# Optimization experiments

Measured on AMD Instinct MI355X. Metric: run time of the kernel, lower is better.

## Reference

```python
import jax, jax.numpy as jnp
import numpy as np

NTASKS = 10
CAP = 8
L = 256
D_IN = 768
D_DOWN = 768
B = 64
NUM_ITERS = 3


def squash(t, axis=-1, eps=1e-16):
    sq = jnp.sum(t * t, axis=axis, keepdims=True) + eps
    return (sq / (1.0 + sq)) * t / jnp.sqrt(sq)


def setup_inputs() -> dict:
    key = jax.random.key(0)
    ks = jax.random.split(key, 8)
    return {
        "x": jax.random.normal(ks[0], (B, L, D_IN), jnp.float32),
        "fc1_w": jax.random.normal(ks[1], (NTASKS, D_DOWN, D_IN), jnp.float32) * 0.02,
        "fc1_b": jax.random.normal(ks[2], (NTASKS, D_DOWN), jnp.float32) * 0.02,
        "fc2_w": jax.random.normal(ks[3], (NTASKS, CAP, D_DOWN), jnp.float32) * 0.02,
        "fc2_b": jax.random.normal(ks[4], (NTASKS, CAP), jnp.float32) * 0.02,
        "route_weights": jax.random.normal(ks[5], (CAP, NTASKS, L * CAP, L), jnp.float32),
        "larger_w": jax.random.normal(ks[6], (NTASKS, D_DOWN, CAP), jnp.float32) * 0.02,
        "larger_b": jax.random.normal(ks[7], (NTASKS, D_DOWN), jnp.float32) * 0.02,
        "eval_t": 5,
    }


def reference(x, fc1_w, fc1_b, fc2_w, fc2_b, route_weights, larger_w, larger_b, eval_t):
    # ---- semantic capsules: per-task two-layer MLP ----
    # h1: [T, B, L, D_DOWN]; h2: [T, B, L, CAP]
    h1 = jnp.einsum("bli,tdi->tbld", x, fc1_w) + fc1_b[:, None, None, :]
    h2 = jnp.einsum("tbld,tcd->tblc", h1, fc2_w) + fc2_b[:, None, None, :]
    # torch: per-task view(B, L*CAP, 1) then cat on last dim -> [B, L*CAP, T]
    sem = jnp.transpose(h2.reshape(NTASKS, B, L * CAP), (1, 2, 0))
    sem = squash(sem, axis=-1)            # squash over task dim (dim=-1)
    sem = jnp.transpose(sem, (0, 2, 1))   # [B, T, L*CAP]

    # ---- tsv capsules: dynamic routing ----
    # priors: [CAP, B, T, class_dim=L]  (singleton dim of torch version dropped)
    priors = jnp.einsum("bri,crio->cbro", sem, route_weights)
    tsv_row = (jnp.arange(NTASKS) <= eval_t).astype(priors.dtype)   # tril row
    mask = jnp.where(tsv_row > 0, 0.0, -10000.0).astype(priors.dtype)
    logits = jnp.zeros_like(priors)
    vote = None
    for i in range(NUM_ITERS):
        logits = logits * tsv_row[None, None, :, None] + mask[None, None, :, None]
        probs = jax.nn.softmax(logits, axis=2)               # over routes (tasks)
        vote = jnp.sum(probs * priors, axis=2, keepdims=True)  # [CAP, B, 1, L]
        out = squash(vote, axis=-1)
        if i != NUM_ITERS - 1:
            logits = logits + jnp.sum(priors * out, axis=-1, keepdims=True)

    # torch raw view: [CAP, B, 1, 1, L] flat -> (B, L, CAP)
    h = vote.reshape(B, L, CAP)
    h = jnp.einsum("blc,dc->bld", h, larger_w[eval_t]) + larger_b[eval_t]
    return h


if __name__ == "__main__":
    out = reference(**setup_inputs())
    print(out.shape)
```

## Files before the change

### kernel.cpp

```cpp
#include <hip/hip_runtime.h>

constexpr int NT = 10;
constexpr int CP = 8;
constexpr int LLn = 256;
constexpr int DI = 768;
constexpr int DD = 768;
constexpr int BB = 64;
constexpr int BLr = BB * LLn;
constexpr int RR = LLn * CP;

__global__ __launch_bounds__(256) void k_w12(const float* __restrict__ w1,
                                             const float* __restrict__ w2,
                                             float* __restrict__ w12) {
  const int t = blockIdx.y;
  const int i0 = blockIdx.x * 64;
  __shared__ float sW1[64][68];
  __shared__ float sW2[CP][64];
  const int tid = threadIdx.x;
  const int il = tid >> 2;
  const int cc = (tid & 3) * 2;
  float a0 = 0.f, a1 = 0.f;
  for (int d0 = 0; d0 < DD; d0 += 64) {
#pragma unroll
    for (int p = 0; p < 4; p++) {
      int idx = p * 256 + tid;
      int dl = idx >> 4, c4 = (idx & 15) * 4;
      *(float4*)&sW1[dl][c4] =
          *(const float4*)(w1 + ((size_t)t * DD + d0 + dl) * DI + i0 + c4);
    }
    if (tid < 128) {
      int c = tid >> 4, d4 = (tid & 15) * 4;
      *(float4*)&sW2[c][d4] =
          *(const float4*)(w2 + ((size_t)t * CP + c) * DD + d0 + d4);
    }
    __syncthreads();
#pragma unroll 16
    for (int dl = 0; dl < 64; ++dl) {
      float v = sW1[dl][il];
      a0 += v * sW2[cc][dl];
      a1 += v * sW2[cc + 1][dl];
    }
    __syncthreads();
  }
  w12[((size_t)t * CP + cc) * DI + i0 + il]     = a0;
  w12[((size_t)t * CP + cc + 1) * DI + i0 + il] = a1;
}

__global__ __launch_bounds__(128) void k_b12(const float* __restrict__ b1,
                                             const float* __restrict__ w2,
                                             const float* __restrict__ b2,
                                             float* __restrict__ b12) {
  int tc = threadIdx.x;
  if (tc >= NT * CP) return;
  int t = tc >> 3, c = tc & 7;
  float s = b2[t * CP + c];
  const float* b1r = b1 + (size_t)t * DD;
  const float* w2r = w2 + ((size_t)t * CP + c) * DD;
  for (int d = 0; d < DD; ++d) s += b1r[d] * w2r[d];
  b12[tc] = s;
}

__global__ __launch_bounds__(256) void k_fc(const float* __restrict__ x,
                                            const float* __restrict__ w12,
                                            const float* __restrict__ b12,
                                            float* __restrict__ h2) {
  const int m0 = blockIdx.x * 64;
  const int tid = threadIdx.x;
  const int q = tid & 7;
  const int mg = tid >> 3;
  const float4* x4 = (const float4*)x;
  const float4* w4 = (const float4*)w12;
  const float4* xr0 = x4 + (size_t)(m0 + 2 * mg) * (DI / 4);
  const float4* xr1 = xr0 + (DI / 4);
  const float4* wr = w4 + (size_t)(q * 10) * (DI / 4);
  float acc0[10], acc1[10];
#pragma unroll
  for (int k = 0; k < 10; ++k) { acc0[k] = 0.f; acc1[k] = 0.f; }
#pragma unroll 2
  for (int i4 = 0; i4 < DI / 4; ++i4) {
    float4 xv0 = xr0[i4];
    float4 xv1 = xr1[i4];
#pragma unroll
    for (int k = 0; k < 10; ++k) {
      float4 wv = wr[(size_t)k * (DI / 4) + i4];
      acc0[k] += xv0.x * wv.x + xv0.y * wv.y + xv0.z * wv.z + xv0.w * wv.w;
      acc1[k] += xv1.x * wv.x + xv1.y * wv.y + xv1.z * wv.z + xv1.w * wv.w;
    }
  }
#pragma unroll
  for (int k = 0; k < 10; ++k) {
    int tc = q * 10 + k;
    int t = tc >> 3, c = tc & 7;
    float bv = b12[tc];
    h2[((size_t)t * BLr + m0 + 2 * mg + 0) * CP + c] = acc0[k] + bv;
    h2[((size_t)t * BLr + m0 + 2 * mg + 1) * CP + c] = acc1[k] + bv;
  }
}

__global__ __launch_bounds__(256) void k_squash_sem(const float* __restrict__ h2,
                                                    const int* __restrict__ etp,
                                                    float* __restrict__ sems) {
  int et = *etp;
  int i = blockIdx.x * 256 + threadIdx.x;
  if (i >= BB * RR) return;
  float v[NT];
  float sq = 0.f;
#pragma unroll
  for (int t = 0; t < NT; ++t) {
    v[t] = h2[(size_t)t * BB * RR + i];
    sq += v[t] * v[t];
  }
  sq += 1e-16f;
  float scale = (sq / (1.f + sq)) * rsqrtf(sq);
#pragma unroll
  for (int t = 0; t < NT; ++t)
    if (t <= et) sems[(size_t)t * BB * RR + i] = scale * v[t];
}

constexpr int OT = 64;
constexpr int RK = 64;
__global__ __launch_bounds__(256) void k_priors(const float* __restrict__ sems,
                                                const float* __restrict__ rw,
                                                const int* __restrict__ etp,
                                                float* __restrict__ priors) {
  int et = *etp;
  int t = blockIdx.y;
  if (t > et) return;
  int c2 = blockIdx.z;
  int o0 = blockIdx.x * OT;
  int tid = threadIdx.x;
  __shared__ float semT[RK][BB + 4];
  __shared__ float rwS[RK][OT + 4];
  int og = (tid & 15) * 4;
  int bg = (tid >> 4) * 4;
  float acc[4][4] = {};
  for (int r0 = 0; r0 < RR; r0 += RK) {
#pragma unroll
    for (int p = 0; p < 4; p++) {
      int idx = p * 256 + tid;
      int b = idx >> 4;
      int r4 = (idx & 15) * 4;
      float4 v = *(const float4*)(sems + ((size_t)t * BB + b) * RR + r0 + r4);
      semT[r4 + 0][b] = v.x; semT[r4 + 1][b] = v.y;
      semT[r4 + 2][b] = v.z; semT[r4 + 3][b] = v.w;
    }
#pragma unroll
    for (int p = 0; p < 4; p++) {
      int idx = p * 256 + tid;
      int r = idx >> 4;
      int o4 = (idx & 15) * 4;
      *(float4*)&rwS[r][o4] =
          *(const float4*)(rw + ((size_t)(c2 * NT + t) * RR + r0 + r) * LLn + o0 + o4);
    }
    __syncthreads();
#pragma unroll 8
    for (int r = 0; r < RK; ++r) {
      float4 a = *(const float4*)&semT[r][bg];
      float4 w = *(const float4*)&rwS[r][og];
#pragma unroll
      for (int i = 0; i < 4; i++)
#pragma unroll
        for (int j = 0; j < 4; j++) acc[i][j] += a[i] * w[j];
    }
    __syncthreads();
  }
#pragma unroll
  for (int i = 0; i < 4; i++)
#pragma unroll
    for (int j = 0; j < 4; j++)
      priors[((size_t)(c2 * NT + t) * BB + bg + i) * LLn + o0 + og + j] = acc[i][j];
}

__global__ __launch_bounds__(256) void k_route(const float* __restrict__ priors,
                                               const int* __restrict__ etp,
                                               float* __restrict__ h) {
  int et = *etp;
  int b = blockIdx.x, c2 = blockIdx.y;
  int o = threadIdx.x;
  __shared__ float pri[NT][LLn];
  __shared__ float rbuf[256];
  for (int t = 0; t <= et; ++t)
    pri[t][o] = priors[((size_t)(c2 * NT + t) * BB + b) * LLn + o];
  __syncthreads();
  float Lg[NT];
#pragma unroll
  for (int t = 0; t < NT; ++t) Lg[t] = 0.f;
  float vote = 0.f;
  for (int it = 0; it < 3; ++it) {
    float mx = -1e30f;
    for (int t = 0; t <= et; ++t) mx = fmaxf(mx, Lg[t]);
    float p[NT];
    float s = 0.f;
    for (int t = 0; t <= et; ++t) { p[t] = expf(Lg[t] - mx); s += p[t]; }
    float inv = 1.f / s;
    vote = 0.f;
    for (int t = 0; t <= et; ++t) vote += p[t] * inv * pri[t][o];
    if (it == 2) break;
    rbuf[o] = vote * vote;
    __syncthreads();
    for (int st = 128; st > 0; st >>= 1) {
      if (o < st) rbuf[o] += rbuf[o + st];
      __syncthreads();
    }
    float sq = rbuf[0] + 1e-16f;
    __syncthreads();
    float scale = (sq / (1.f + sq)) * rsqrtf(sq);
    for (int t = 0; t <= et; ++t) {
      rbuf[o] = pri[t][o] * vote;
      __syncthreads();
      for (int st = 128; st > 0; st >>= 1) {
        if (o < st) rbuf[o] += rbuf[o + st];
        __syncthreads();
      }
      Lg[t] += scale * rbuf[0];
      __syncthreads();
    }
  }
  h[((size_t)c2 * BB + b) * LLn + o] = vote;
}

__global__ __launch_bounds__(256) void k_out(const float* __restrict__ h,
                                             const float* __restrict__ lw,
                                             const float* __restrict__ lb,
                                             const int* __restrict__ etp,
                                             float* __restrict__ out) {
  int et = *etp;
  int row = blockIdx.x;
  const float* hr = h + (size_t)row * CP;
  float hv[CP];
#pragma unroll
  for (int c = 0; c < CP; ++c) hv[c] = hr[c];
  const float* lwb = lw + (size_t)et * DD * CP;
  const float* lbb = lb + (size_t)et * DD;
  for (int d = threadIdx.x; d < DD; d += 256) {
    const float* w = lwb + (size_t)d * CP;
    float s2 = lbb[d];
#pragma unroll
    for (int c = 0; c < CP; ++c) s2 += hv[c] * w[c];
    out[(size_t)row * DD + d] = s2;
  }
}

extern "C" void kernel_launch(void* const* d_in, const int* in_sizes, int n_in,
                              void* d_out, int out_size, void* d_ws, size_t ws_size,
                              hipStream_t stream) {
  const float* x  = (const float*)d_in[0];
  const float* w1 = (const float*)d_in[1];
  const float* b1 = (const float*)d_in[2];
  const float* w2 = (const float*)d_in[3];
  const float* b2 = (const float*)d_in[4];
  const float* rw = (const float*)d_in[5];
  const float* lw = (const float*)d_in[6];
  const float* lb = (const float*)d_in[7];
  const int* etp  = (const int*)d_in[8];
  float* out = (float*)d_out;

  char* ws = (char*)d_ws;
  size_t off = 0;
  auto alloc = [&](size_t bytes) {
    void* p = ws + off;
    off = (off + bytes + 255) & ~(size_t)255;
    return p;
  };
  float* w12   = (float*)alloc((size_t)NT * CP * DI * 4);
  float* b12   = (float*)alloc((size_t)NT * CP * 4);
  float* h2    = (float*)alloc((size_t)NT * BLr * CP * 4);
  float* sems  = (float*)alloc((size_t)NT * BB * RR * 4);
  float* priors= (float*)alloc((size_t)CP * NT * BB * LLn * 4);
  float* hbuf  = (float*)alloc((size_t)CP * BB * LLn * 4);

  k_w12<<<dim3(DI / 64, NT), 256, 0, stream>>>(w1, w2, w12);
  k_b12<<<1, 128, 0, stream>>>(b1, w2, b2, b12);
  k_fc<<<BLr / 64, 256, 0, stream>>>(x, w12, b12, h2);
  k_squash_sem<<<(BB * RR + 255) / 256, 256, 0, stream>>>(h2, etp, sems);
  k_priors<<<dim3(LLn / OT, NT, CP), 256, 0, stream>>>(sems, rw, etp, priors);
  k_route<<<dim3(BB, CP), 256, 0, stream>>>(priors, etp, hbuf);
  k_out<<<BLr, 256, 0, stream>>>(hbuf, lw, lb, etp, out);
}
```

Before: 687.5 us.

## Tile fc GEMM through LDS, parallelize bias fold, use wave-level routing

The fused fc kernel now stages x and w12 tiles in double-buffered shared memory with 512 threads, instead of streaming them from global memory per thread. The bias fold kernel spreads each dot product across a 64-lane wavefront with float4 loads and a shuffle reduction. The routing kernel drops from 256 threads with shared-memory tree reductions to a single wavefront per (batch, capsule), keeping priors in registers and reducing with __shfl_xor. These changes target global-load inefficiency and synchronisation overhead, at the cost of more LDS use and register pressure in k_fc.

```diff
diff --git a/kernel.cpp b/kernel.cpp
--- a/kernel.cpp
+++ b/kernel.cpp
@@ -46,54 +46,92 @@
   w12[((size_t)t * CP + cc + 1) * DI + i0 + il] = a1;
 }
 
-__global__ __launch_bounds__(128) void k_b12(const float* __restrict__ b1,
+__global__ __launch_bounds__(256) void k_b12(const float* __restrict__ b1,
                                              const float* __restrict__ w2,
                                              const float* __restrict__ b2,
                                              float* __restrict__ b12) {
-  int tc = threadIdx.x;
-  if (tc >= NT * CP) return;
-  int t = tc >> 3, c = tc & 7;
-  float s = b2[t * CP + c];
+  const int tc = blockIdx.x * 4 + (threadIdx.x >> 6);
+  const int lane = threadIdx.x & 63;
+  const int t = tc >> 3, c = tc & 7;
   const float* b1r = b1 + (size_t)t * DD;
   const float* w2r = w2 + ((size_t)t * CP + c) * DD;
-  for (int d = 0; d < DD; ++d) s += b1r[d] * w2r[d];
-  b12[tc] = s;
-}
-
-__global__ __launch_bounds__(256) void k_fc(const float* __restrict__ x,
+  float s = 0.f;
+  for (int d = lane * 4; d < DD; d += 256) {
+    float4 bv = *(const float4*)(b1r + d);
+    float4 wv = *(const float4*)(w2r + d);
+    s += bv.x * wv.x + bv.y * wv.y + bv.z * wv.z + bv.w * wv.w;
+  }
+#pragma unroll
+  for (int st = 32; st > 0; st >>= 1) s += __shfl_xor(s, st, 64);
+  if (lane == 0) b12[tc] = s + b2[t * CP + c];
+}
+
+__global__ __launch_bounds__(512) void k_fc(const float* __restrict__ x,
                                             const float* __restrict__ w12,
                                             const float* __restrict__ b12,
                                             float* __restrict__ h2) {
+  __shared__ float xs[2][64][68];
+  __shared__ float ws[2][80][68];
+  const int tid = threadIdx.x;
   const int m0 = blockIdx.x * 64;
-  const int tid = threadIdx.x;
-  const int q = tid & 7;
-  const int mg = tid >> 3;
-  const float4* x4 = (const float4*)x;
-  const float4* w4 = (const float4*)w12;
-  const float4* xr0 = x4 + (size_t)(m0 + 2 * mg) * (DI / 4);
-  const float4* xr1 = xr0 + (DI / 4);
-  const float4* wr = w4 + (size_t)(q * 10) * (DI / 4);
-  float acc0[10], acc1[10];
-#pragma unroll
-  for (int k = 0; k < 10; ++k) { acc0[k] = 0.f; acc1[k] = 0.f; }
-#pragma unroll 2
-  for (int i4 = 0; i4 < DI / 4; ++i4) {
-    float4 xv0 = xr0[i4];
-    float4 xv1 = xr1[i4];
-#pragma unroll
-    for (int k = 0; k < 10; ++k) {
-      float4 wv = wr[(size_t)k * (DI / 4) + i4];
-      acc0[k] += xv0.x * wv.x + xv0.y * wv.y + xv0.z * wv.z + xv0.w * wv.w;
-      acc1[k] += xv1.x * wv.x + xv1.y * wv.y + xv1.z * wv.z + xv1.w * wv.w;
-    }
-  }
-#pragma unroll
-  for (int k = 0; k < 10; ++k) {
-    int tc = q * 10 + k;
+  const int q  = tid & 15;
+  const int mg = tid >> 4;
+
+  const int srow = tid >> 4;
+  const int scol = (tid & 15) * 4;
+  const float* xg = x + (size_t)(m0 + srow) * DI + (tid & 15) * 4;
+  const float* wg = w12 + (size_t)srow * DI + (tid & 15) * 4;
+
+  float4 xr[2], wr[3];
+  float acc0[5] = {}, acc1[5] = {};
+
+  auto GLOAD = [&](int k0) {
+    xr[0] = *(const float4*)(xg + k0);
+    xr[1] = *(const float4*)(xg + (size_t)32 * DI + k0);
+    wr[0] = *(const float4*)(wg + k0);
+    wr[1] = *(const float4*)(wg + (size_t)32 * DI + k0);
+    if (tid < 256) wr[2] = *(const float4*)(wg + (size_t)64 * DI + k0);
+  };
+  auto WRITE = [&](int buf) {
+    *(float4*)&xs[buf][srow][scol]      = xr[0];
+    *(float4*)&xs[buf][32 + srow][scol] = xr[1];
+    *(float4*)&ws[buf][srow][scol]      = wr[0];
+    *(float4*)&ws[buf][32 + srow][scol] = wr[1];
+    if (tid < 256) *(float4*)&ws[buf][64 + srow][scol] = wr[2];
+  };
+
+  GLOAD(0);
+  WRITE(0);
+  __syncthreads();
+
+  for (int s = 0; s < 12; ++s) {
+    if (s < 11) GLOAD((s + 1) * 64);
+    const int buf = s & 1;
+#pragma unroll
+    for (int k4 = 0; k4 < 16; ++k4) {
+      float4 xv0 = *(const float4*)&xs[buf][2 * mg + 0][k4 * 4];
+      float4 xv1 = *(const float4*)&xs[buf][2 * mg + 1][k4 * 4];
+#pragma unroll
+      for (int kk = 0; kk < 5; ++kk) {
+        float4 wv = *(const float4*)&ws[buf][q + 16 * kk][k4 * 4];
+        acc0[kk] += xv0.x * wv.x + xv0.y * wv.y + xv0.z * wv.z + xv0.w * wv.w;
+        acc1[kk] += xv1.x * wv.x + xv1.y * wv.y + xv1.z * wv.z + xv1.w * wv.w;
+      }
+    }
+    if (s < 11) {
+      WRITE((s + 1) & 1);
+      __syncthreads();
+    }
+  }
+
+#pragma unroll
+  for (int kk = 0; kk < 5; ++kk) {
+    int tc = q + 16 * kk;
     int t = tc >> 3, c = tc & 7;
     float bv = b12[tc];
-    h2[((size_t)t * BLr + m0 + 2 * mg + 0) * CP + c] = acc0[k] + bv;
-    h2[((size_t)t * BLr + m0 + 2 * mg + 1) * CP + c] = acc1[k] + bv;
+    size_t base = ((size_t)t * BLr + m0 + 2 * mg) * CP + c;
+    h2[base]      = acc0[kk] + bv;
+    h2[base + CP] = acc1[kk] + bv;
   }
 }
 
@@ -171,52 +209,78 @@
       priors[((size_t)(c2 * NT + t) * BB + bg + i) * LLn + o0 + og + j] = acc[i][j];
 }
 
-__global__ __launch_bounds__(256) void k_route(const float* __restrict__ priors,
-                                               const int* __restrict__ etp,
-                                               float* __restrict__ h) {
-  int et = *etp;
-  int b = blockIdx.x, c2 = blockIdx.y;
-  int o = threadIdx.x;
-  __shared__ float pri[NT][LLn];
-  __shared__ float rbuf[256];
-  for (int t = 0; t <= et; ++t)
-    pri[t][o] = priors[((size_t)(c2 * NT + t) * BB + b) * LLn + o];
-  __syncthreads();
+__global__ __launch_bounds__(64) void k_route(const float* __restrict__ priors,
+                                              const int* __restrict__ etp,
+                                              float* __restrict__ h) {
+  const int et = *etp;
+  const int b = blockIdx.x >> 3;
+  const int c2 = blockIdx.x & 7;
+  const int lane = threadIdx.x;
+
+  float pri[NT][4];
+#pragma unroll
+  for (int t = 0; t < NT; ++t) {
+    if (t <= et) {
+#pragma unroll
+      for (int j = 0; j < 4; ++j)
+        pri[t][j] = priors[((size_t)(c2 * NT + t) * BB + b) * LLn + j * 64 + lane];
+    } else {
+#pragma unroll
+      for (int j = 0; j < 4; ++j) pri[t][j] = 0.f;
+    }
+  }
+
   float Lg[NT];
 #pragma unroll
   for (int t = 0; t < NT; ++t) Lg[t] = 0.f;
-  float vote = 0.f;
+  float vote[4] = {};
+
   for (int it = 0; it < 3; ++it) {
     float mx = -1e30f;
-    for (int t = 0; t <= et; ++t) mx = fmaxf(mx, Lg[t]);
+#pragma unroll
+    for (int t = 0; t < NT; ++t)
+      if (t <= et) mx = fmaxf(mx, Lg[t]);
     float p[NT];
     float s = 0.f;
-    for (int t = 0; t <= et; ++t) { p[t] = expf(Lg[t] - mx); s += p[t]; }
+#pragma unroll
+    for (int t = 0; t < NT; ++t) {
+      p[t] = (t <= et) ? __expf(Lg[t] - mx) : 0.f;
+      s += p[t];
+    }
     float inv = 1.f / s;
-    vote = 0.f;
-    for (int t = 0; t <= et; ++t) vote += p[t] * inv * pri[t][o];
+#pragma unroll
+    for (int j = 0; j < 4; ++j) vote[j] = 0.f;
+#pragma unroll
+    for (int t = 0; t < NT; ++t) {
+      if (t <= et) {
+        float w = p[t] * inv;
+#pragma unroll
+        for (int j = 0; j < 4; ++j) vote[j] += w * pri[t][j];
+      }
+    }
     if (it == 2) break;
-    rbuf[o] = vote * vote;
-    __syncthreads();
-    for (int st = 128; st > 0; st >>= 1) {
-      if (o < st) rbuf[o] += rbuf[o + st];
-      __syncthreads();
-    }
-    float sq = rbuf[0] + 1e-16f;
-    __syncthreads();
+
+    float sq = vote[0] * vote[0] + vote[1] * vote[1] + vote[2] * vote[2] + vote[3] * vote[3];
+#pragma unroll
+    for (int st = 32; st > 0; st >>= 1) sq += __shfl_xor(sq, st, 64);
+    sq += 1e-16f;
     float scale = (sq / (1.f + sq)) * rsqrtf(sq);
-    for (int t = 0; t <= et; ++t) {
-      rbuf[o] = pri[t][o] * vote;
-      __syncthreads();
-      for (int st = 128; st > 0; st >>= 1) {
-        if (o < st) rbuf[o] += rbuf[o + st];
-        __syncthreads();
+
+#pragma unroll
+    for (int t = 0; t < NT; ++t) {
+      if (t <= et) {
+        float dot = pri[t][0] * vote[0] + pri[t][1] * vote[1] +
+                    pri[t][2] * vote[2] + pri[t][3] * vote[3];
+#pragma unroll
+        for (int st = 32; st > 0; st >>= 1) dot += __shfl_xor(dot, st, 64);
+        Lg[t] += scale * dot;
       }
-      Lg[t] += scale * rbuf[0];
-      __syncthreads();
-    }
-  }
-  h[((size_t)c2 * BB + b) * LLn + o] = vote;
+    }
+  }
+
+#pragma unroll
+  for (int j = 0; j < 4; ++j)
+    h[((size_t)c2 * BB + b) * LLn + j * 64 + lane] = vote[j];
 }
 
 __global__ __launch_bounds__(256) void k_out(const float* __restrict__ h,
@@ -270,10 +334,10 @@
   float* hbuf  = (float*)alloc((size_t)CP * BB * LLn * 4);
 
   k_w12<<<dim3(DI / 64, NT), 256, 0, stream>>>(w1, w2, w12);
-  k_b12<<<1, 128, 0, stream>>>(b1, w2, b2, b12);
-  k_fc<<<BLr / 64, 256, 0, stream>>>(x, w12, b12, h2);
+  k_b12<<<20, 256, 0, stream>>>(b1, w2, b2, b12);
+  k_fc<<<BLr / 64, 512, 0, stream>>>(x, w12, b12, h2);
   k_squash_sem<<<(BB * RR + 255) / 256, 256, 0, stream>>>(h2, etp, sems);
   k_priors<<<dim3(LLn / OT, NT, CP), 256, 0, stream>>>(sems, rw, etp, priors);
-  k_route<<<dim3(BB, CP), 256, 0, stream>>>(priors, etp, hbuf);
+  k_route<<<BB * CP, 64, 0, stream>>>(priors, etp, hbuf);
   k_out<<<BLr, 256, 0, stream>>>(hbuf, lw, lb, etp, out);
 }
```

New measurement: 938.2 us. 36.5% more time.
